# Performance work log

Hardware: AMD Instinct MI355X
Metric: run time of the kernel (lower is better)

## Reference

```python
import jax, jax.numpy as jnp
import numpy as np

NB_ATOMS = 128
NB_CH = 1
ATOM = 12          # atom_size
BATCH = 8
HW = 75            # -> 64x64 patch grid
LAM = 0.1          # soft-threshold level of the L1 proximal
UNROLL = 2         # unroll_steps
FISTA_ITERS = 15   # fixed inner FISTA iterations (replaces res-based stop)


def _prox(u):
    # soft-thresholding (prox of lam*||.||_1)
    return jnp.sign(u) * jnp.maximum(jnp.abs(u) - LAM, 0.0)


def _conv(x, w):
    # valid cross-correlation, NCHW / OIHW (== F.conv2d)
    return jax.lax.conv_general_dilated(x, w, (1, 1), 'VALID',
                                        dimension_numbers=('NCHW', 'OIHW', 'NCHW'))


def _fold(patches, H, W):
    # patches: [B, Ph, Pw, a, a] -> overlap-add to [B, 1, H, W] (== F.fold)
    B, Ph, Pw, a, _ = patches.shape
    out = jnp.zeros((B, H, W), patches.dtype)
    for di in range(a):              # fixed small kernel loop (a*a = 144 slots)
        for dj in range(a):
            out = out.at[:, di:di + Ph, dj:dj + Pw].add(patches[:, :, :, di, dj])
    return out[:, None]


def _fista(c0, X, q, mu):
    # standard FISTA on 0.5*||D^T c - y_patch||^2 + lam*||c||_1 with step mu
    def body(i, st):
        c, z, t = st
        cn = _prox(z - (z @ X - q) * mu)
        tn = (1.0 + jnp.sqrt(1.0 + 4.0 * t * t)) / 2.0
        zn = cn + ((t - 1.0) / tn) * (cn - c)
        return (cn, zn, tn)
    c, _, _ = jax.lax.fori_loop(0, FISTA_ITERS, body, (c0, c0, jnp.float32(1.0)))
    return c


def setup_inputs() -> dict:
    key = jax.random.key(0)
    k1, k2 = jax.random.split(key)
    y = jax.random.normal(k1, (BATCH, NB_CH, HW, HW), dtype=jnp.float32)
    atoms = jax.random.normal(k2, (NB_ATOMS, NB_CH, ATOM, ATOM), dtype=jnp.float32) / 1500.0
    beta = jnp.float32(0.1)
    mu = jnp.float32(1.0)
    return {"y": y, "atoms": atoms, "beta": beta, "mu": mu}


def reference(y, atoms, beta, mu):
    B, C, H, W = y.shape
    N, a = atoms.shape[0], atoms.shape[-1]
    beta = jax.nn.relu(beta)
    mu = jax.nn.relu(mu)
    # normalize atoms: zero-mean, unit L2 rows, then spectral norm / sqrt(mu)
    A = atoms - atoms.mean(axis=(1, 2, 3), keepdims=True)
    Af = A.reshape(N, -1)
    Af = Af / jnp.linalg.norm(Af, axis=1, keepdims=True)
    Af = Af / (jnp.linalg.norm(Af, ord=2) * jnp.sqrt(mu))
    atoms_n = Af.reshape(N, C, a, a)
    X = Af @ Af.T                                   # [N, N] gram
    Ph, Pw = H - a + 1, W - a + 1
    n_patch = B * Ph * Pw
    mean_filter = jnp.ones((1, 1, a, a), y.dtype) / (a * a)
    patch_mean = _conv(y, mean_filter).reshape(n_patch, 1, 1, 1)
    divisors = _fold(jnp.ones((B, Ph, Pw, a, a), y.dtype), H, W)  # overlap counts
    goal = y
    c = jnp.zeros((n_patch, N), y.dtype)
    sg = jax.lax.stop_gradient
    for _ in range(UNROLL):
        q = _conv(goal, atoms_n).transpose(0, 2, 3, 1).reshape(n_patch, N)
        cf = sg(_fista(sg(c), sg(X), sg(q), sg(mu)))   # torch.no_grad inner solve
        cf = _prox(cf - (cf @ X - q) * mu)             # one differentiable step
        pred = jnp.einsum('pn,ncij->pcij', cf, atoms_n) + patch_mean  # [P,1,a,a]
        pred = _fold(pred.reshape(B, Ph, Pw, a, a), H, W)
        goal = (y + beta * pred) / (1.0 + beta * divisors)
        c = cf
    return goal
```

## Files before the change

### kernel.cpp

```cpp
#include <hip/hip_runtime.h>
#include <stdint.h>

#define AA 144
#define LAM 0.1f

#define OFS_SC    0
#define OFS_AF1   64
#define OFS_G     36928
#define OFS_S0    53312
#define OFS_S1    69696
#define OFS_X     86080
#define OFS_PM    139328
#define OFS_GOAL  172096
#define OFS_CF    4411456
#define OFS_PRED  8605760
#define OFS_ATB   OFS_S0
#define OFS_ANTB  OFS_S1


typedef __attribute__((ext_vector_type(8))) short short8_t;
typedef __attribute__((ext_vector_type(4))) float f32x4;
typedef __attribute__((ext_vector_type(4))) uint32_t u32x4;

__device__ __forceinline__ unsigned short f2bf(float f) {
    union { float f; uint32_t u; } x; x.f = f;
    uint32_t u = x.u;
    return (unsigned short)((u + 0x7FFFu + ((u >> 16) & 1u)) >> 16);
}
__device__ __forceinline__ unsigned short f2bh(float f) {
    union { float f; uint32_t u; } x; x.f = f;
    return (unsigned short)((x.u + 0x8000u) >> 16);
}
__device__ __forceinline__ float bf2f(unsigned short u) {
    union { float f; uint32_t i; } x; x.i = ((uint32_t)u) << 16; return x.f;
}
__device__ __forceinline__ uint32_t pack_bf(float a, float b) {
    union { float f; uint32_t u; } xa, xb; xa.f = a; xb.f = b;
    return __builtin_amdgcn_perm(xb.u + 0x8000u, xa.u + 0x8000u, 0x07060302u);
}
__device__ __forceinline__ uint32_t cvt_pk(float a, float b) {
    uint32_t r;
    asm("v_cvt_pk_bf16_f32 %0, %1, %2" : "=v"(r) : "v"(a), "v"(b));
    return r;
}

#define PSTR 136
__global__ __launch_bounds__(1024) void k_setup(const float* atoms, const float* mu_p,
                                                float* ws, const float* y) {
    __shared__ unsigned short ABf[128 * 168];
    __shared__ unsigned short Pb[2][128 * PSTR];
    __shared__ float tr_arr[10];
    __shared__ float v[128];
    __shared__ float red[256];
    int t = threadIdx.x;
    if (blockIdx.x != 0) {
        int e = (blockIdx.x - 1) * 1024 + t;
        if (e < 45000) ws[OFS_GOAL + e] = y[e];
        if (e < 32768) {
            int b = e >> 12, pi = (e >> 6) & 63, pj = e & 63;
            const float* yb = y + b * 5625;
            float s = 0.f;
            for (int di = 0; di < 12; ++di) {
                const float* row = yb + (pi + di) * 75 + pj;
                #pragma unroll
                for (int dj = 0; dj < 12; ++dj) s += row[dj];
            }
            ws[OFS_PM + e] = s * (1.0f / 144.0f);
        }
        return;
    }
    int lane = t & 63, w = t >> 6;
    int col = lane & 15, quad = lane >> 4;
    if (t < 10) tr_arr[t] = (t == 0) ? 128.0f : 0.f;

    {
        int a = t >> 3, sub = t & 7;
        const float* ap = atoms + a * AA + sub * 18;
        float s = 0.f;
        #pragma unroll
        for (int k = 0; k < 18; ++k) s += ap[k];
        s += __shfl_xor(s, 1, 8); s += __shfl_xor(s, 2, 8); s += __shfl_xor(s, 4, 8);
        float mean = s * (1.0f / 144.0f);
        float ss = 0.f;
        #pragma unroll
        for (int k = 0; k < 18; ++k) { float d = ap[k] - mean; ss = fmaf(d, d, ss); }
        ss += __shfl_xor(ss, 1, 8); ss += __shfl_xor(ss, 2, 8); ss += __shfl_xor(ss, 4, 8);
        float rn = 1.0f / sqrtf(ss);
        #pragma unroll
        for (int k = 0; k < 18; ++k) {
            float av = (ap[k] - mean) * rn;
            ws[OFS_AF1 + a * AA + sub * 18 + k] = av;
            ABf[a * 168 + sub * 18 + k] = f2bf(av);
        }
        if (sub == 0) {
            #pragma unroll
            for (int k = AA; k < 160; ++k) ABf[a * 168 + k] = 0;
        }
    }
    __syncthreads();

    {
        uint32_t* D32 = (uint32_t*)Pb[0];
        float* G = ws + OFS_G;
        int mt = w & 7, gh = w >> 3;
        short8_t af[5];
        #pragma unroll
        for (int s = 0; s < 5; ++s)
            af[s] = *(const short8_t*)&ABf[(mt * 16 + col) * 168 + s * 32 + quad * 8];
        #pragma unroll
        for (int gi = 0; gi < 2; ++gi) {
            int g = gh * 2 + gi;
            short8_t b0[5], b1[5];
            #pragma unroll
            for (int s = 0; s < 5; ++s) {
                b0[s] = *(const short8_t*)&ABf[((2 * g) * 16 + col) * 168 + s * 32 + quad * 8];
                b1[s] = *(const short8_t*)&ABf[((2 * g + 1) * 16 + col) * 168 + s * 32 + quad * 8];
            }
            f32x4 a0 = (f32x4){0.f, 0.f, 0.f, 0.f};
            f32x4 a1 = (f32x4){0.f, 0.f, 0.f, 0.f};
            #pragma unroll
            for (int s = 0; s < 5; ++s) {
                a0 = __builtin_amdgcn_mfma_f32_16x16x32_bf16(af[s], b0[s], a0, 0, 0, 0);
                a1 = __builtin_amdgcn_mfma_f32_16x16x32_bf16(af[s], b1[s], a1, 0, 0, 0);
            }
            #pragma unroll
            for (int r = 0; r < 4; ++r) {
                int m = mt * 16 + quad * 4 + r;
                G[m * 128 + g * 32 + col] = a0[r];
                G[m * 128 + g * 32 + 16 + col] = a1[r];
                D32[m * 68 + g * 16 + col] = pack_bf(a0[r], a1[r]);
            }
        }
    }
    __syncthreads();

    int cur = 0;
    #pragma unroll 1
    for (int j = 0; j < 8; ++j) {
        float trn = tr_arr[j];
        float inv2 = 1.0f / (trn * trn);
        const unsigned short* S = Pb[cur];
        uint32_t* D32 = (uint32_t*)Pb[cur ^ 1];
        int mt = w & 7, nh = w >> 3;
        short8_t af[4];
        #pragma unroll
        for (int s = 0; s < 4; ++s)
            af[s] = *(const short8_t*)&S[(mt * 16 + col) * PSTR + s * 32 + quad * 8];
        #pragma unroll
        for (int pr = 0; pr < 2; ++pr) {
            int ntE = 4 * nh + 2 * pr, ntO = ntE + 1;
            short8_t bE[4], bO[4];
            #pragma unroll
            for (int s = 0; s < 4; ++s) {
                bE[s] = *(const short8_t*)&S[(ntE * 16 + col) * PSTR + s * 32 + quad * 8];
                bO[s] = *(const short8_t*)&S[(ntO * 16 + col) * PSTR + s * 32 + quad * 8];
            }
            f32x4 aE = (f32x4){0.f, 0.f, 0.f, 0.f};
            f32x4 aO = (f32x4){0.f, 0.f, 0.f, 0.f};
            #pragma unroll
            for (int s = 0; s < 4; ++s) {
                aE = __builtin_amdgcn_mfma_f32_16x16x32_bf16(af[s], bE[s], aE, 0, 0, 0);
                aO = __builtin_amdgcn_mfma_f32_16x16x32_bf16(af[s], bO[s], aO, 0, 0, 0);
            }
            int nE = ntE * 16 + col, nO = ntO * 16 + col;
            #pragma unroll
            for (int r = 0; r < 4; ++r) {
                float x0 = aE[r] * inv2, x1 = aO[r] * inv2;
                int row = mt * 16 + quad * 4 + r;
                D32[row * 68 + (ntE >> 1) * 16 + col] = pack_bf(x0, x1);
                if (row == nE) atomicAdd(&tr_arr[j + 1], x0);
                if (row == nO) atomicAdd(&tr_arr[j + 1], x1);
            }
        }
        __syncthreads();
        cur ^= 1;
    }

    {
        int a = t >> 3, sub = t & 7;
        const unsigned short* S = Pb[cur];
        float s = 0.f;
        #pragma unroll
        for (int k = 0; k < 16; ++k) s += bf2f(S[a * PSTR + sub * 16 + k]);
        s += __shfl_xor(s, 1, 8); s += __shfl_xor(s, 2, 8); s += __shfl_xor(s, 4, 8);
        if (sub == 0) v[a] = s;
    }
    __syncthreads();
    {
        int a = t >> 3, sub = t & 7;
        const float* G = ws + OFS_G;
        float wv = 0.f;
        #pragma unroll
        for (int k = 0; k < 16; ++k)
            wv = fmaf(G[a * 128 + sub * 16 + k], v[sub * 16 + k], wv);
        wv += __shfl_xor(wv, 1, 8); wv += __shfl_xor(wv, 2, 8); wv += __shfl_xor(wv, 4, 8);
        if (sub == 0) { red[a] = v[a] * wv; red[128 + a] = v[a] * v[a]; }
    }
    __syncthreads();
    for (int off = 64; off > 0; off >>= 1) {
        if (t < off) { red[t] += red[t + off]; red[128 + t] += red[128 + t + off]; }
        __syncthreads();
    }
    if (t == 0) {
        float lam = red[0] / red[128];
        float mu = fmaxf(mu_p[0], 0.0f);
        float scX = 1.0f / (lam * mu);
        float scA = 1.0f / (sqrtf(lam) * sqrtf(mu));
        ws[OFS_SC + 16] = scX * mu;
        ws[OFS_SC + 17] = scA;
        ws[OFS_SC + 18] = -scA * mu;
    }
}

__global__ __launch_bounds__(256) void k_finalize(float* ws) {
    int idx = blockIdx.x * 256 + threadIdx.x;
    float scX = ws[OFS_SC + 16], scA = ws[OFS_SC + 17], scQ = ws[OFS_SC + 18];
    if (idx < 16384) {
        int row = idx >> 7, ks = idx & 127;
        int s = ks >> 5, Q = (ks >> 3) & 3, j = ks & 7;
        int n = 32 * s + 16 * (j >> 2) + 4 * Q + (j & 3);
        ((unsigned short*)(ws + OFS_X))[idx] = f2bf(ws[OFS_G + row * 128 + n] * scX);
    } else if (idx < 36864) {
        int e = idx - 16384;
        int n = e / 160, k = e - n * 160;
        float v = (k < 144) ? ws[OFS_AF1 + n * 144 + k] * scQ : 0.f;
        ((unsigned short*)(ws + OFS_ATB))[e] = f2bf(v);
    } else {
        int e = idx - 36864;
        int jr = e >> 7, ks = e & 127;
        int s = ks >> 5, Q = (ks >> 3) & 3, j = ks & 7;
        int n = 32 * s + 16 * (j >> 2) + 4 * Q + (j & 3);
        ((unsigned short*)(ws + OFS_ANTB))[e] = f2bf(ws[OFS_AF1 + n * 144 + jr] * scA);
    }
}

__global__ __launch_bounds__(128, 3) void k_fista(const unsigned short* XPB,
        const float* goal, const unsigned short* ATB, const unsigned short* ANTBP,
        const float* pm, uint32_t* cfgb, unsigned short* predh,
        int first, int write_cf) {
    __shared__ u32x4 Zx[2][2][2][64];
    int t = threadIdx.x;
    int lane = t & 63, w = t >> 6;
    int ow = w ^ 1;
    int col = lane & 15, Q = lane >> 4;
    int so0 = 2 * w, so1 = 2 * w + 1;
    int sx0 = 2 * ow, sx1 = 2 * ow + 1;
    int blk = blockIdx.x;
    int b = blk >> 8, pi = (blk >> 2) & 63;
    int pcol = (blk & 3) * 16 + col;
    int p = blk * 16 + col;
    const float* gb = goal + b * 5625 + pi * 75;

    u32x4 bq[5];
    #pragma unroll
    for (int s = 0; s < 5; ++s)
        #pragma unroll
        for (int jj = 0; jj < 4; ++jj) {
            int k0 = 32 * s + 8 * Q + 2 * jj;
            float v0 = 0.f, v1 = 0.f;
            if (k0 < 144) {
                int di = k0 / 12, dj = k0 - di * 12;
                const float* r = gb + di * 75 + pcol + dj;
                v0 = r[0]; v1 = r[1];
            }
            bq[s][jj] = cvt_pk(v0, v1);
        }

    f32x4 qn4[4];
    #pragma unroll
    for (int m = 0; m < 4; ++m) {
        short8_t af[5];
        #pragma unroll
        for (int s = 0; s < 5; ++s)
            af[s] = *(const short8_t*)&ATB[((w * 4 + m) * 16 + col) * 160 + 32 * s + 8 * Q];
        f32x4 a = (f32x4){0.f, 0.f, 0.f, 0.f};
        #pragma unroll
        for (int s = 0; s < 5; ++s)
            a = __builtin_amdgcn_mfma_f32_16x16x32_bf16(af[s],
                    __builtin_bit_cast(short8_t, bq[s]), a, 0, 0, 0);
        qn4[m] = a;
    }

    short8_t xfo[4][2], xfx[4][2];
    #pragma unroll
    for (int m = 0; m < 4; ++m) {
        const unsigned short* Xr = &XPB[((w * 4 + m) * 16 + col) * 128 + 8 * Q];
        xfo[m][0] = *(const short8_t*)&Xr[32 * so0];
        xfo[m][1] = *(const short8_t*)&Xr[32 * so1];
        xfx[m][0] = *(const short8_t*)&Xr[32 * sx0];
        xfx[m][1] = *(const short8_t*)&Xr[32 * sx1];
    }

    f32x4 c4[4], z4[4], acc4[4];
    u32x4 own0, own1, oth0, oth1;
    if (first) {
        #pragma unroll
        for (int m = 0; m < 4; ++m) c4[m] = z4[m] = (f32x4){0.f, 0.f, 0.f, 0.f};
        own0 = own1 = oth0 = oth1 = (u32x4){0u, 0u, 0u, 0u};
    } else {
        const u32x4* cp = (const u32x4*)(cfgb + ((size_t)blk * 64 + lane) * 16);
        own0 = cp[so0]; own1 = cp[so1];
        oth0 = cp[sx0]; oth1 = cp[sx1];
        #pragma unroll
        for (int jj = 0; jj < 4; ++jj) {
            int m = jj >> 1, r = 2 * (jj & 1);
            uint32_t p0 = own0[jj], p1 = own1[jj];
            c4[m][r]         = __builtin_bit_cast(float, p0 << 16);
            c4[m][r + 1]     = __builtin_bit_cast(float, p0 & 0xFFFF0000u);
            c4[2 + m][r]     = __builtin_bit_cast(float, p1 << 16);
            c4[2 + m][r + 1] = __builtin_bit_cast(float, p1 & 0xFFFF0000u);
        }
        #pragma unroll
        for (int m = 0; m < 4; ++m) z4[m] = c4[m];
    }

    auto matmul = [&]() {
        #pragma unroll
        for (int m = 0; m < 4; ++m)
            acc4[m] = __builtin_amdgcn_mfma_f32_16x16x32_bf16(xfo[m][0],
                          __builtin_bit_cast(short8_t, own0), qn4[m], 0, 0, 0);
        #pragma unroll
        for (int m = 0; m < 4; ++m)
            acc4[m] = __builtin_amdgcn_mfma_f32_16x16x32_bf16(xfo[m][1],
                          __builtin_bit_cast(short8_t, own1), acc4[m], 0, 0, 0);
        #pragma unroll
        for (int m = 0; m < 4; ++m)
            acc4[m] = __builtin_amdgcn_mfma_f32_16x16x32_bf16(xfx[m][0],
                          __builtin_bit_cast(short8_t, oth0), acc4[m], 0, 0, 0);
        #pragma unroll
        for (int m = 0; m < 4; ++m)
            acc4[m] = __builtin_amdgcn_mfma_f32_16x16x32_bf16(xfx[m][1],
                          __builtin_bit_cast(short8_t, oth1), acc4[m], 0, 0, 0);
    };
    auto pack = [&](f32x4 (&src)[4]) {
        #pragma unroll
        for (int jj = 0; jj < 4; ++jj) {
            int m = jj >> 1, r = 2 * (jj & 1);
            own0[jj] = cvt_pk(src[m][r], src[m][r + 1]);
            own1[jj] = cvt_pk(src[2 + m][r], src[2 + m][r + 1]);
        }
    };
    auto exchange = [&](int buf) {
        Zx[buf][w][0][lane] = own0;
        Zx[buf][w][1][lane] = own1;
        __syncthreads();
        oth0 = Zx[buf][ow][0][lane];
        oth1 = Zx[buf][ow][1][lane];
    };

    float tm = 1.0f;
    #pragma unroll 2
    for (int it = 0; it < 14; ++it) {
        matmul();
        float tn = 0.5f * (1.0f + sqrtf(1.0f + 4.0f * tm * tm));
        float fm = (tm - 1.0f) / tn;
        tm = tn;
        f32x4 fm4 = (f32x4){fm, fm, fm, fm};
        #pragma unroll
        for (int m = 0; m < 4; ++m) {
            f32x4 u = z4[m] - acc4[m];
            f32x4 cl;
            #pragma unroll
            for (int e = 0; e < 4; ++e) cl[e] = __builtin_amdgcn_fmed3f(u[e], -LAM, LAM);
            f32x4 cn = u - cl;
            z4[m] = cn + fm4 * (cn - c4[m]);
            c4[m] = cn;
        }
        pack(z4);
        exchange(it & 1);
    }
    {
        matmul();
        #pragma unroll
        for (int m = 0; m < 4; ++m) {
            f32x4 u = z4[m] - acc4[m];
            f32x4 cl;
            #pragma unroll
            for (int e = 0; e < 4; ++e) cl[e] = __builtin_amdgcn_fmed3f(u[e], -LAM, LAM);
            c4[m] = u - cl;
        }
        pack(c4);
        exchange(0);
    }
    {
        matmul();
        #pragma unroll
        for (int m = 0; m < 4; ++m) {
            f32x4 u = c4[m] - acc4[m];
            f32x4 cl;
            #pragma unroll
            for (int e = 0; e < 4; ++e) cl[e] = __builtin_amdgcn_fmed3f(u[e], -LAM, LAM);
            c4[m] = u - cl;
        }
        pack(c4);
        exchange(1);
    }
    if (write_cf) {
        u32x4* cp = (u32x4*)(cfgb + ((size_t)blk * 64 + lane) * 16);
        cp[so0] = own0;
        cp[so1] = own1;
    }

    {
        float pmv = pm[p];
        f32x4 pm4 = (f32x4){pmv, pmv, pmv, pmv};
        int jm0 = w ? 5 : 0, jmN = w ? 4 : 5;
        #pragma unroll
        for (int ji = 0; ji < 5; ++ji) {
            if (ji < jmN) {
                int jm = jm0 + ji;
                const unsigned short* Ar = &ANTBP[(jm * 16 + col) * 128 + 8 * Q];
                short8_t ao0 = *(const short8_t*)&Ar[32 * so0];
                short8_t ao1 = *(const short8_t*)&Ar[32 * so1];
                short8_t ax0 = *(const short8_t*)&Ar[32 * sx0];
                short8_t ax1 = *(const short8_t*)&Ar[32 * sx1];
                f32x4 a = pm4;
                a = __builtin_amdgcn_mfma_f32_16x16x32_bf16(ao0,
                        __builtin_bit_cast(short8_t, own0), a, 0, 0, 0);
                a = __builtin_amdgcn_mfma_f32_16x16x32_bf16(ao1,
                        __builtin_bit_cast(short8_t, own1), a, 0, 0, 0);
                a = __builtin_amdgcn_mfma_f32_16x16x32_bf16(ax0,
                        __builtin_bit_cast(short8_t, oth0), a, 0, 0, 0);
                a = __builtin_amdgcn_mfma_f32_16x16x32_bf16(ax1,
                        __builtin_bit_cast(short8_t, oth1), a, 0, 0, 0);
                #pragma unroll
                for (int r = 0; r < 4; ++r)
                    predh[(jm * 16 + 4 * Q + r) * 32768 + p] = f2bh(a[r]);
            }
        }
    }
}

__global__ __launch_bounds__(256) void k_fold(const float* y, const float* beta_p,
                                              const unsigned short* predh, float* goal,
                                              float* out, int write_out) {
    __shared__ float P[12 * 832];
    int i = blockIdx.x, b = blockIdx.y;
    int t = threadIdx.x;
    for (int di = 0; di < 12; ++di) {
        int pi = i - di;
        if ((unsigned)pi >= 64u) continue;
        int base = (b << 12) + (pi << 6);
        #pragma unroll
        for (int it = 0; it < 3; ++it) {
            int e = t + it * 256;
            int dj = e >> 6, pj = e & 63;
            P[di * 832 + pj * 13 + dj] = bf2f(predh[(di * 12 + dj) * 32768 + base + pj]);
        }
    }
    __syncthreads();
    if (t >= 75) return;
    int j = t;
    float S = 0.f;
    for (int di = 0; di < 12; ++di) {
        if ((unsigned)(i - di) >= 64u) continue;
        const float* Pd = &P[di * 832];
        #pragma unroll
        for (int dj = 0; dj < 12; ++dj) {
            int pj = j - dj;
            if ((unsigned)pj >= 64u) continue;
            S += Pd[pj * 13 + dj];
        }
    }
    int ci = min(i, 11) - max(i - 63, 0) + 1;
    int cj = min(j, 11) - max(j - 63, 0) + 1;
    float beta = fmaxf(beta_p[0], 0.0f);
    int idx = i * 75 + j;
    float yv = y[b * 5625 + idx];
    float g = (yv + beta * S) / (1.0f + beta * (float)(ci * cj));
    if (write_out) out[b * 5625 + idx] = g;
    else           goal[b * 5625 + idx] = g;
}

extern "C" void kernel_launch(void* const* d_in, const int* in_sizes, int n_in,
                              void* d_out, int out_size, void* d_ws, size_t ws_size,
                              hipStream_t stream) {
    const float* y     = (const float*)d_in[0];
    const float* atoms = (const float*)d_in[1];
    const float* beta  = (const float*)d_in[2];
    const float* mu    = (const float*)d_in[3];
    float* out = (float*)d_out;
    float* ws = (float*)d_ws;

    k_setup<<<46, 1024, 0, stream>>>(atoms, mu, ws, y);
    k_finalize<<<216, 256, 0, stream>>>(ws);

    for (int u = 0; u < 2; ++u) {
        k_fista<<<2048, 128, 0, stream>>>((const unsigned short*)(ws + OFS_X),
                                          ws + OFS_GOAL,
                                          (const unsigned short*)(ws + OFS_ATB),
                                          (const unsigned short*)(ws + OFS_ANTB),
                                          ws + OFS_PM, (uint32_t*)(ws + OFS_CF),
                                          (unsigned short*)(ws + OFS_PRED),
                                          u == 0 ? 1 : 0, u == 0 ? 1 : 0);
        k_fold<<<dim3(75, 8), 256, 0, stream>>>(y, beta,
                                                (const unsigned short*)(ws + OFS_PRED),
                                                ws + OFS_GOAL, out, u == 1 ? 1 : 0);
    }
}
```

Measured before the change: 201.2 us.

## Process two 16-patch tiles per FISTA block to reuse Gram fragments

Each k_fista block now handles 32 patches (two independent 16-column tiles A and B) instead of 16, halving the grid to 1024 blocks. The X Gram fragments and atom fragments loaded into registers are shared across both tiles, and the two interleaved MFMA chains give the scheduler independent work to hide MFMA latency, while one barrier per iteration now covers both tiles. The cost is higher register pressure (launch bounds lowered from 3 to 2 waves-per-EU hint) and fewer blocks, which could reduce occupancy and latency hiding. The inner loop unroll drops from 2 to 1.

```diff
diff --git a/kernel.cpp b/kernel.cpp
--- a/kernel.cpp
+++ b/kernel.cpp
@@ -234,11 +234,11 @@
     }
 }
 
-__global__ __launch_bounds__(128, 3) void k_fista(const unsigned short* XPB,
+__global__ __launch_bounds__(128, 2) void k_fista(const unsigned short* XPB,
         const float* goal, const unsigned short* ATB, const unsigned short* ANTBP,
         const float* pm, uint32_t* cfgb, unsigned short* predh,
         int first, int write_cf) {
-    __shared__ u32x4 Zx[2][2][2][64];
+    __shared__ u32x4 Zx[2][2][2][2][64];
     int t = threadIdx.x;
     int lane = t & 63, w = t >> 6;
     int ow = w ^ 1;
@@ -246,39 +246,43 @@
     int so0 = 2 * w, so1 = 2 * w + 1;
     int sx0 = 2 * ow, sx1 = 2 * ow + 1;
     int blk = blockIdx.x;
-    int b = blk >> 8, pi = (blk >> 2) & 63;
-    int pcol = (blk & 3) * 16 + col;
-    int p = blk * 16 + col;
+    int b = blk >> 7, pi = (blk >> 1) & 63;
+    int pcA = (blk & 1) * 32 + col;
+    int pA = blk * 32 + col, pB = pA + 16;
     const float* gb = goal + b * 5625 + pi * 75;
 
-    u32x4 bq[5];
+    u32x4 bqA[5], bqB[5];
     #pragma unroll
     for (int s = 0; s < 5; ++s)
         #pragma unroll
         for (int jj = 0; jj < 4; ++jj) {
             int k0 = 32 * s + 8 * Q + 2 * jj;
-            float v0 = 0.f, v1 = 0.f;
+            float a0 = 0.f, a1 = 0.f, b0 = 0.f, b1 = 0.f;
             if (k0 < 144) {
                 int di = k0 / 12, dj = k0 - di * 12;
-                const float* r = gb + di * 75 + pcol + dj;
-                v0 = r[0]; v1 = r[1];
-            }
-            bq[s][jj] = cvt_pk(v0, v1);
-        }
-
-    f32x4 qn4[4];
+                const float* r = gb + di * 75 + pcA + dj;
+                a0 = r[0]; a1 = r[1];
+                b0 = r[16]; b1 = r[17];
+            }
+            bqA[s][jj] = cvt_pk(a0, a1);
+            bqB[s][jj] = cvt_pk(b0, b1);
+        }
+
+    f32x4 qnA[4], qnB[4];
     #pragma unroll
     for (int m = 0; m < 4; ++m) {
-        short8_t af[5];
-        #pragma unroll
-        for (int s = 0; s < 5; ++s)
-            af[s] = *(const short8_t*)&ATB[((w * 4 + m) * 16 + col) * 160 + 32 * s + 8 * Q];
-        f32x4 a = (f32x4){0.f, 0.f, 0.f, 0.f};
-        #pragma unroll
-        for (int s = 0; s < 5; ++s)
-            a = __builtin_amdgcn_mfma_f32_16x16x32_bf16(af[s],
-                    __builtin_bit_cast(short8_t, bq[s]), a, 0, 0, 0);
-        qn4[m] = a;
+        f32x4 aA = (f32x4){0.f, 0.f, 0.f, 0.f};
+        f32x4 aB = (f32x4){0.f, 0.f, 0.f, 0.f};
+        #pragma unroll
+        for (int s = 0; s < 5; ++s) {
+            short8_t af = *(const short8_t*)&ATB[((w * 4 + m) * 16 + col) * 160 + 32 * s + 8 * Q];
+            aA = __builtin_amdgcn_mfma_f32_16x16x32_bf16(af,
+                     __builtin_bit_cast(short8_t, bqA[s]), aA, 0, 0, 0);
+            aB = __builtin_amdgcn_mfma_f32_16x16x32_bf16(af,
+                     __builtin_bit_cast(short8_t, bqB[s]), aB, 0, 0, 0);
+        }
+        qnA[m] = aA;
+        qnB[m] = aB;
     }
 
     short8_t xfo[4][2], xfx[4][2];
@@ -291,70 +295,60 @@
         xfx[m][1] = *(const short8_t*)&Xr[32 * sx1];
     }
 
-    f32x4 c4[4], z4[4], acc4[4];
-    u32x4 own0, own1, oth0, oth1;
+    f32x4 cA[4], zA[4], accA[4], cB[4], zB[4], accB[4];
+    u32x4 ownA0, ownA1, othA0, othA1, ownB0, ownB1, othB0, othB1;
     if (first) {
         #pragma unroll
-        for (int m = 0; m < 4; ++m) c4[m] = z4[m] = (f32x4){0.f, 0.f, 0.f, 0.f};
-        own0 = own1 = oth0 = oth1 = (u32x4){0u, 0u, 0u, 0u};
+        for (int m = 0; m < 4; ++m) {
+            cA[m] = zA[m] = (f32x4){0.f, 0.f, 0.f, 0.f};
+            cB[m] = zB[m] = (f32x4){0.f, 0.f, 0.f, 0.f};
+        }
+        ownA0 = ownA1 = othA0 = othA1 = (u32x4){0u, 0u, 0u, 0u};
+        ownB0 = ownB1 = othB0 = othB1 = (u32x4){0u, 0u, 0u, 0u};
     } else {
-        const u32x4* cp = (const u32x4*)(cfgb + ((size_t)blk * 64 + lane) * 16);
-        own0 = cp[so0]; own1 = cp[so1];
-        oth0 = cp[sx0]; oth1 = cp[sx1];
+        const u32x4* cpA = (const u32x4*)(cfgb + ((size_t)(2 * blk) * 64 + lane) * 16);
+        const u32x4* cpB = (const u32x4*)(cfgb + ((size_t)(2 * blk + 1) * 64 + lane) * 16);
+        ownA0 = cpA[so0]; ownA1 = cpA[so1]; othA0 = cpA[sx0]; othA1 = cpA[sx1];
+        ownB0 = cpB[so0]; ownB1 = cpB[so1]; othB0 = cpB[sx0]; othB1 = cpB[sx1];
         #pragma unroll
         for (int jj = 0; jj < 4; ++jj) {
             int m = jj >> 1, r = 2 * (jj & 1);
-            uint32_t p0 = own0[jj], p1 = own1[jj];
-            c4[m][r]         = __builtin_bit_cast(float, p0 << 16);
-            c4[m][r + 1]     = __builtin_bit_cast(float, p0 & 0xFFFF0000u);
-            c4[2 + m][r]     = __builtin_bit_cast(float, p1 << 16);
-            c4[2 + m][r + 1] = __builtin_bit_cast(float, p1 & 0xFFFF0000u);
-        }
-        #pragma unroll
-        for (int m = 0; m < 4; ++m) z4[m] = c4[m];
-    }
-
-    auto matmul = [&]() {
+            uint32_t a0 = ownA0[jj], a1 = ownA1[jj];
+            cA[m][r]         = __builtin_bit_cast(float, a0 << 16);
+            cA[m][r + 1]     = __builtin_bit_cast(float, a0 & 0xFFFF0000u);
+            cA[2 + m][r]     = __builtin_bit_cast(float, a1 << 16);
+            cA[2 + m][r + 1] = __builtin_bit_cast(float, a1 & 0xFFFF0000u);
+            uint32_t b0 = ownB0[jj], b1 = ownB1[jj];
+            cB[m][r]         = __builtin_bit_cast(float, b0 << 16);
+            cB[m][r + 1]     = __builtin_bit_cast(float, b0 & 0xFFFF0000u);
+            cB[2 + m][r]     = __builtin_bit_cast(float, b1 << 16);
+            cB[2 + m][r + 1] = __builtin_bit_cast(float, b1 & 0xFFFF0000u);
+        }
+        #pragma unroll
+        for (int m = 0; m < 4; ++m) { zA[m] = cA[m]; zB[m] = cB[m]; }
+    }
+
+    auto matmul = [&](u32x4& o0, u32x4& o1, u32x4& x0, u32x4& x1,
+                      f32x4 (&qn)[4], f32x4 (&acc)[4]) {
         #pragma unroll
         for (int m = 0; m < 4; ++m)
-            acc4[m] = __builtin_amdgcn_mfma_f32_16x16x32_bf16(xfo[m][0],
-                          __builtin_bit_cast(short8_t, own0), qn4[m], 0, 0, 0);
+            acc[m] = __builtin_amdgcn_mfma_f32_16x16x32_bf16(xfo[m][0],
+                         __builtin_bit_cast(short8_t, o0), qn[m], 0, 0, 0);
         #pragma unroll
         for (int m = 0; m < 4; ++m)
-            acc4[m] = __builtin_amdgcn_mfma_f32_16x16x32_bf16(xfo[m][1],
-                          __builtin_bit_cast(short8_t, own1), acc4[m], 0, 0, 0);
+            acc[m] = __builtin_amdgcn_mfma_f32_16x16x32_bf16(xfo[m][1],
+                         __builtin_bit_cast(short8_t, o1), acc[m], 0, 0, 0);
         #pragma unroll
         for (int m = 0; m < 4; ++m)
-            acc4[m] = __builtin_amdgcn_mfma_f32_16x16x32_bf16(xfx[m][0],
-                          __builtin_bit_cast(short8_t, oth0), acc4[m], 0, 0, 0);
+            acc[m] = __builtin_amdgcn_mfma_f32_16x16x32_bf16(xfx[m][0],
+                         __builtin_bit_cast(short8_t, x0), acc[m], 0, 0, 0);
         #pragma unroll
         for (int m = 0; m < 4; ++m)
-            acc4[m] = __builtin_amdgcn_mfma_f32_16x16x32_bf16(xfx[m][1],
-                          __builtin_bit_cast(short8_t, oth1), acc4[m], 0, 0, 0);
+            acc[m] = __builtin_amdgcn_mfma_f32_16x16x32_bf16(xfx[m][1],
+                         __builtin_bit_cast(short8_t, x1), acc[m], 0, 0, 0);
     };
-    auto pack = [&](f32x4 (&src)[4]) {
-        #pragma unroll
-        for (int jj = 0; jj < 4; ++jj) {
-            int m = jj >> 1, r = 2 * (jj & 1);
-            own0[jj] = cvt_pk(src[m][r], src[m][r + 1]);
-            own1[jj] = cvt_pk(src[2 + m][r], src[2 + m][r + 1]);
-        }
-    };
-    auto exchange = [&](int buf) {
-        Zx[buf][w][0][lane] = own0;
-        Zx[buf][w][1][lane] = own1;
-        __syncthreads();
-        oth0 = Zx[buf][ow][0][lane];
-        oth1 = Zx[buf][ow][1][lane];
-    };
-
-    float tm = 1.0f;
-    #pragma unroll 2
-    for (int it = 0; it < 14; ++it) {
-        matmul();
-        float tn = 0.5f * (1.0f + sqrtf(1.0f + 4.0f * tm * tm));
-        float fm = (tm - 1.0f) / tn;
-        tm = tn;
+    auto do_iter = [&](f32x4 (&c4)[4], f32x4 (&z4)[4], f32x4 (&acc4)[4],
+                       u32x4& o0, u32x4& o1, float fm) {
         f32x4 fm4 = (f32x4){fm, fm, fm, fm};
         #pragma unroll
         for (int m = 0; m < 4; ++m) {
@@ -366,44 +360,79 @@
             z4[m] = cn + fm4 * (cn - c4[m]);
             c4[m] = cn;
         }
-        pack(z4);
-        exchange(it & 1);
-    }
-    {
-        matmul();
+        #pragma unroll
+        for (int jj = 0; jj < 4; ++jj) {
+            int m = jj >> 1, r = 2 * (jj & 1);
+            o0[jj] = cvt_pk(z4[m][r], z4[m][r + 1]);
+            o1[jj] = cvt_pk(z4[2 + m][r], z4[2 + m][r + 1]);
+        }
+    };
+    auto do_prox = [&](f32x4 (&base)[4], f32x4 (&c4)[4], f32x4 (&acc4)[4],
+                       u32x4& o0, u32x4& o1) {
         #pragma unroll
         for (int m = 0; m < 4; ++m) {
-            f32x4 u = z4[m] - acc4[m];
+            f32x4 u = base[m] - acc4[m];
             f32x4 cl;
             #pragma unroll
             for (int e = 0; e < 4; ++e) cl[e] = __builtin_amdgcn_fmed3f(u[e], -LAM, LAM);
             c4[m] = u - cl;
         }
-        pack(c4);
+        #pragma unroll
+        for (int jj = 0; jj < 4; ++jj) {
+            int m = jj >> 1, r = 2 * (jj & 1);
+            o0[jj] = cvt_pk(c4[m][r], c4[m][r + 1]);
+            o1[jj] = cvt_pk(c4[2 + m][r], c4[2 + m][r + 1]);
+        }
+    };
+    auto exchange = [&](int buf) {
+        Zx[buf][0][w][0][lane] = ownA0;
+        Zx[buf][0][w][1][lane] = ownA1;
+        Zx[buf][1][w][0][lane] = ownB0;
+        Zx[buf][1][w][1][lane] = ownB1;
+        __syncthreads();
+        othA0 = Zx[buf][0][ow][0][lane];
+        othA1 = Zx[buf][0][ow][1][lane];
+        othB0 = Zx[buf][1][ow][0][lane];
+        othB1 = Zx[buf][1][ow][1][lane];
+    };
+
+    float tm = 1.0f;
+    #pragma unroll 1
+    for (int it = 0; it < 14; ++it) {
+        matmul(ownA0, ownA1, othA0, othA1, qnA, accA);
+        matmul(ownB0, ownB1, othB0, othB1, qnB, accB);
+        float tn = 0.5f * (1.0f + sqrtf(1.0f + 4.0f * tm * tm));
+        float fm = (tm - 1.0f) / tn;
+        tm = tn;
+        do_iter(cA, zA, accA, ownA0, ownA1, fm);
+        do_iter(cB, zB, accB, ownB0, ownB1, fm);
+        exchange(it & 1);
+    }
+    {
+        matmul(ownA0, ownA1, othA0, othA1, qnA, accA);
+        matmul(ownB0, ownB1, othB0, othB1, qnB, accB);
+        do_prox(zA, cA, accA, ownA0, ownA1);
+        do_prox(zB, cB, accB, ownB0, ownB1);
         exchange(0);
     }
     {
-        matmul();
-        #pragma unroll
-        for (int m = 0; m < 4; ++m) {
-            f32x4 u = c4[m] - acc4[m];
-            f32x4 cl;
-            #pragma unroll
-            for (int e = 0; e < 4; ++e) cl[e] = __builtin_amdgcn_fmed3f(u[e], -LAM, LAM);
-            c4[m] = u - cl;
-        }
-        pack(c4);
+        matmul(ownA0, ownA1, othA0, othA1, qnA, accA);
+        matmul(ownB0, ownB1, othB0, othB1, qnB, accB);
+        do_prox(cA, cA, accA, ownA0, ownA1);
+        do_prox(cB, cB, accB, ownB0, ownB1);
         exchange(1);
     }
     if (write_cf) {
-        u32x4* cp = (u32x4*)(cfgb + ((size_t)blk * 64 + lane) * 16);
-        cp[so0] = own0;
-        cp[so1] = own1;
-    }
-
-    {
-        float pmv = pm[p];
-        f32x4 pm4 = (f32x4){pmv, pmv, pmv, pmv};
+        u32x4* cpA = (u32x4*)(cfgb + ((size_t)(2 * blk) * 64 + lane) * 16);
+        u32x4* cpB = (u32x4*)(cfgb + ((size_t)(2 * blk + 1) * 64 + lane) * 16);
+        cpA[so0] = ownA0; cpA[so1] = ownA1;
+        cpB[so0] = ownB0; cpB[so1] = ownB1;
+    }
+
+    {
+        float pmA = pm[pA], pmB = pm[pB];
+        f32x4 pmA4 = (f32x4){pmA, pmA, pmA, pmA};
+        f32x4 pmB4 = (f32x4){pmB, pmB, pmB, pmB};
         int jm0 = w ? 5 : 0, jmN = w ? 4 : 5;
         #pragma unroll
         for (int ji = 0; ji < 5; ++ji) {
@@ -414,18 +443,29 @@
                 short8_t ao1 = *(const short8_t*)&Ar[32 * so1];
                 short8_t ax0 = *(const short8_t*)&Ar[32 * sx0];
                 short8_t ax1 = *(const short8_t*)&Ar[32 * sx1];
-                f32x4 a = pm4;
+                f32x4 a = pmA4;
                 a = __builtin_amdgcn_mfma_f32_16x16x32_bf16(ao0,
-                        __builtin_bit_cast(short8_t, own0), a, 0, 0, 0);
+                        __builtin_bit_cast(short8_t, ownA0), a, 0, 0, 0);
                 a = __builtin_amdgcn_mfma_f32_16x16x32_bf16(ao1,
-                        __builtin_bit_cast(short8_t, own1), a, 0, 0, 0);
+                        __builtin_bit_cast(short8_t, ownA1), a, 0, 0, 0);
                 a = __builtin_amdgcn_mfma_f32_16x16x32_bf16(ax0,
-                        __builtin_bit_cast(short8_t, oth0), a, 0, 0, 0);
+                        __builtin_bit_cast(short8_t, othA0), a, 0, 0, 0);
                 a = __builtin_amdgcn_mfma_f32_16x16x32_bf16(ax1,
-                        __builtin_bit_cast(short8_t, oth1), a, 0, 0, 0);
+                        __builtin_bit_cast(short8_t, othA1), a, 0, 0, 0);
+                f32x4 bb = pmB4;
+                bb = __builtin_amdgcn_mfma_f32_16x16x32_bf16(ao0,
+                         __builtin_bit_cast(short8_t, ownB0), bb, 0, 0, 0);
+                bb = __builtin_amdgcn_mfma_f32_16x16x32_bf16(ao1,
+                         __builtin_bit_cast(short8_t, ownB1), bb, 0, 0, 0);
+                bb = __builtin_amdgcn_mfma_f32_16x16x32_bf16(ax0,
+                         __builtin_bit_cast(short8_t, othB0), bb, 0, 0, 0);
+                bb = __builtin_amdgcn_mfma_f32_16x16x32_bf16(ax1,
+                         __builtin_bit_cast(short8_t, othB1), bb, 0, 0, 0);
                 #pragma unroll
-                for (int r = 0; r < 4; ++r)
-                    predh[(jm * 16 + 4 * Q + r) * 32768 + p] = f2bh(a[r]);
+                for (int r = 0; r < 4; ++r) {
+                    predh[(jm * 16 + 4 * Q + r) * 32768 + pA] = f2bh(a[r]);
+                    predh[(jm * 16 + 4 * Q + r) * 32768 + pB] = f2bh(bb[r]);
+                }
             }
         }
     }
@@ -486,7 +526,7 @@
     k_finalize<<<216, 256, 0, stream>>>(ws);
 
     for (int u = 0; u < 2; ++u) {
-        k_fista<<<2048, 128, 0, stream>>>((const unsigned short*)(ws + OFS_X),
+        k_fista<<<1024, 128, 0, stream>>>((const unsigned short*)(ws + OFS_X),
                                           ws + OFS_GOAL,
                                           (const unsigned short*)(ws + OFS_ATB),
                                           (const unsigned short*)(ws + OFS_ANTB),
```

New measurement: 187.3 us. 1.07x faster.
